# Kernel tuning notes

Hardware: AMD Instinct MI355X
Metric: run time of the kernel (lower is better)

## Reference

```python
import jax, jax.numpy as jnp
import numpy as np

HEADS = 4
DIM_HEAD = 32
SCALE = 10.0
EPS = 1e-12  # F.normalize eps


def setup_inputs() -> dict:
    key = jax.random.key(0)
    k0, k1, k2 = jax.random.split(key, 3)
    b, c, h, w = 4, 256, 64, 64
    hidden = HEADS * DIM_HEAD  # 128
    x = jax.random.normal(k0, (b, c, h, w), dtype=jnp.float32)
    # 1x1 convs == per-pixel linear layers; store as [out_ch, in_ch]
    w_qkv = jax.random.normal(k1, (3 * hidden, c), dtype=jnp.float32) * (1.0 / np.sqrt(c))
    w_out = jax.random.normal(k2, (c, hidden), dtype=jnp.float32) * (1.0 / np.sqrt(hidden))
    b_out = jnp.zeros((c,), dtype=jnp.float32)
    return {"x": x, "w_qkv": w_qkv, "w_out": w_out, "b_out": b_out}


def _l2norm(t):
    # normalize along the per-head feature dim d (axis=2 of [b,h,d,n])
    n = jnp.sqrt(jnp.sum(t * t, axis=2, keepdims=True))
    return t / jnp.maximum(n, EPS)


def reference(x, w_qkv, w_out, b_out):
    b, c, h, w = x.shape
    n = h * w
    # to_qkv 1x1 conv (no bias)
    qkv = jnp.einsum('oc,bchw->bohw', w_qkv, x)          # [b, 3*hidden, h, w]
    qkv = qkv.reshape(b, 3, HEADS, DIM_HEAD, n)          # chunk dim=1 then split heads
    q, k, v = qkv[:, 0], qkv[:, 1], qkv[:, 2]            # each [b, heads, d, n]
    q = _l2norm(q)
    k = _l2norm(k)
    sim = jnp.einsum('bhdi,bhdj->bhij', q, k) * SCALE    # [b, heads, n, n]
    attn = jax.nn.softmax(sim, axis=-1)
    out = jnp.einsum('bhij,bhdj->bhid', attn, v)         # [b, heads, n, d]
    # 'b h (x y) d -> b (h d) x y'
    out = out.transpose(0, 1, 3, 2).reshape(b, HEADS * DIM_HEAD, h, w)
    # to_out 1x1 conv with bias
    return jnp.einsum('oc,bchw->bohw', w_out, out) + b_out[None, :, None, None]
```

## Files before the change

kernel.cpp:

```cpp
#include <hip/hip_runtime.h>
#include <math.h>

#define BB 4
#define CC 256
#define NHEAD 4
#define DH 32
#define NN 4096
#define HID 128

typedef _Float16 f16;
typedef _Float16 f16x8 __attribute__((ext_vector_type(8)));
typedef _Float16 f16x4 __attribute__((ext_vector_type(4)));
typedef float f32x4 __attribute__((ext_vector_type(4)));
typedef unsigned int u32x4 __attribute__((ext_vector_type(4)));

#define QPRESCALE 14.42695041f
#define NSHIFT 14.42695041f

#if __has_builtin(__builtin_amdgcn_exp2f)
#define EXP2F(x) __builtin_amdgcn_exp2f(x)
#else
#define EXP2F(x) __expf((x)*0.6931471805599453f)
#endif

__device__ __forceinline__ f16x8 cvt8(const float* p) {
    float4 a = *(const float4*)p;
    float4 b = *(const float4*)(p + 4);
    f16x8 r;
    r[0] = (f16)a.x; r[1] = (f16)a.y; r[2] = (f16)a.z; r[3] = (f16)a.w;
    r[4] = (f16)b.x; r[5] = (f16)b.y; r[6] = (f16)b.z; r[7] = (f16)b.w;
    return r;
}

#define XROW 40

__global__ __launch_bounds__(256, 4) void qkv_mega(const float* __restrict__ x,
                                                   const float* __restrict__ wq,
                                                   f16* __restrict__ qh,
                                                   f16* __restrict__ kh,
                                                   f16* __restrict__ vh) {
    __shared__ __align__(16) f16 xl[32 * XROW];
    int t = threadIdx.x;
    int wave = t >> 6, lane = t & 63;
    int quad = lane >> 4, col = lane & 15;
    int b = blockIdx.z;
    int i0 = blockIdx.x * 32;
    int o0w = blockIdx.y * 128 + wave * 32;

    int sc = t >> 3;
    int iseg = t & 7;
    const float* xb = x + (size_t)b * CC * NN + i0 + iseg * 4;

    f32x4 c[2][2];
#pragma unroll
    for (int mt = 0; mt < 2; mt++)
#pragma unroll
        for (int nt = 0; nt < 2; nt++) c[mt][nt] = f32x4{0.f, 0.f, 0.f, 0.f};

#pragma unroll
    for (int k0 = 0; k0 < CC; k0 += 32) {
        float4 xv = *(const float4*)(xb + (size_t)(k0 + sc) * NN);
        __syncthreads();
        xl[(iseg * 4 + 0) * XROW + sc] = (f16)xv.x;
        xl[(iseg * 4 + 1) * XROW + sc] = (f16)xv.y;
        xl[(iseg * 4 + 2) * XROW + sc] = (f16)xv.z;
        xl[(iseg * 4 + 3) * XROW + sc] = (f16)xv.w;
        __syncthreads();
        f16x8 bf0 = *(const f16x8*)(xl + (size_t)col * XROW + quad * 8);
        f16x8 bf1 = *(const f16x8*)(xl + (size_t)(16 + col) * XROW + quad * 8);
#pragma unroll
        for (int mt = 0; mt < 2; mt++) {
            f16x8 a = cvt8(wq + (size_t)(o0w + mt * 16 + col) * CC + k0 + quad * 8);
            c[mt][0] = __builtin_amdgcn_mfma_f32_16x16x32_f16(a, bf0, c[mt][0], 0, 0, 0);
            c[mt][1] = __builtin_amdgcn_mfma_f32_16x16x32_f16(a, bf1, c[mt][1], 0, 0, 0);
        }
    }

    if (blockIdx.y < 2) {
        int isQ = (blockIdx.y == 0);
        f16* dst = isQ ? qh : kh;
        int h = wave;
        float pre = isQ ? QPRESCALE : 1.0f;
#pragma unroll
        for (int nt = 0; nt < 2; nt++) {
            float ss = 0.f;
#pragma unroll
            for (int m2 = 0; m2 < 2; m2++)
#pragma unroll
                for (int r = 0; r < 4; r++) {
                    float v = c[m2][nt][r];
                    ss = fmaf(v, v, ss);
                }
            ss += __shfl_xor(ss, 16);
            ss += __shfl_xor(ss, 32);
            float inv = pre / fmaxf(sqrtf(ss), 1e-12f);
            size_t row = ((size_t)(b * 4 + h) * NN + i0 + nt * 16 + col) * 32;
#pragma unroll
            for (int m2 = 0; m2 < 2; m2++) {
                f16x4 st;
#pragma unroll
                for (int r = 0; r < 4; r++) st[r] = (f16)(c[m2][nt][r] * inv);
                *(f16x4*)(dst + row + m2 * 16 + quad * 4) = st;
            }
        }
    } else {
        int h = wave;
#pragma unroll
        for (int nt = 0; nt < 2; nt++) {
            int i = i0 + nt * 16 + col;
#pragma unroll
            for (int m2 = 0; m2 < 2; m2++)
#pragma unroll
                for (int r = 0; r < 4; r++)
                    vh[((size_t)(b * 4 + h) * 32 + m2 * 16 + quad * 4 + r) * NN + i] =
                        (f16)c[m2][nt][r];
        }
    }
}

#define KROW 40
#define VROW 72

__device__ __forceinline__ f16x8 expblk2(f32x4 sa, f32x4 sb) {
    u32x4 w;
    w[0] = __builtin_bit_cast(unsigned int,
            __builtin_amdgcn_cvt_pkrtz(EXP2F(sa[0]), EXP2F(sa[1])));
    w[1] = __builtin_bit_cast(unsigned int,
            __builtin_amdgcn_cvt_pkrtz(EXP2F(sa[2]), EXP2F(sa[3])));
    w[2] = __builtin_bit_cast(unsigned int,
            __builtin_amdgcn_cvt_pkrtz(EXP2F(sb[0]), EXP2F(sb[1])));
    w[3] = __builtin_bit_cast(unsigned int,
            __builtin_amdgcn_cvt_pkrtz(EXP2F(sb[2]), EXP2F(sb[3])));
    return __builtin_bit_cast(f16x8, w);
}

__device__ __forceinline__ void compute_g(const f16* kl, const f16* vl, int jb,
                                          int col, int quad, const f16x8 (&qB)[4],
                                          f32x4 (&o)[4][2], f32x4 (&lf)[4]) {
    f16x8 kA = *(const f16x8*)(kl + (jb + col) * KROW + quad * 8);
    f16x8 kB = *(const f16x8*)(kl + (jb + 16 + col) * KROW + quad * 8);
    f16x8 v0 = *(const f16x8*)(vl + col * VROW + jb + quad * 8);
    f16x8 v1 = *(const f16x8*)(vl + (16 + col) * VROW + jb + quad * 8);
    const f32x4 zs = {-NSHIFT, -NSHIFT, -NSHIFT, -NSHIFT};
    f16 one = (f16)1.0f;
    f16x8 ones = {one, one, one, one, one, one, one, one};
#pragma unroll
    for (int f = 0; f < 4; f++) {
        f32x4 sa = __builtin_amdgcn_mfma_f32_16x16x32_f16(kA, qB[f], zs, 0, 0, 0);
        f32x4 sb = __builtin_amdgcn_mfma_f32_16x16x32_f16(kB, qB[f], zs, 0, 0, 0);
        f16x8 p = expblk2(sa, sb);
        o[f][0] = __builtin_amdgcn_mfma_f32_16x16x32_f16(p, v0, o[f][0], 0, 0, 0);
        o[f][1] = __builtin_amdgcn_mfma_f32_16x16x32_f16(p, v1, o[f][1], 0, 0, 0);
        lf[f]   = __builtin_amdgcn_mfma_f32_16x16x32_f16(p, ones, lf[f], 0, 0, 0);
    }
}

template <int SPLIT>
__global__ __launch_bounds__(256, 4) void attn_mfma(const f16* __restrict__ qh,
                                                    const f16* __restrict__ kh,
                                                    const f16* __restrict__ vh,
                                                    float* __restrict__ op,
                                                    float* __restrict__ lp,
                                                    f16* __restrict__ att16) {
    __shared__ __align__(16) f16 klds[2][64 * KROW];
    __shared__ __align__(16) f16 vlds[2][32 * VROW];
    int t = threadIdx.x;
    int wave = t >> 6, lane = t & 63;
    int quad = lane >> 4, col = lane & 15;

    int bid = blockIdx.x;
    int xcd = bid & 7;
    int slot = bid >> 3;
    int bh = xcd * 2 + slot / (16 * SPLIT);
    int rem = slot % (16 * SPLIT);
    int s = rem >> 4;
    int i0 = (rem & 15) * 256;
    int iw = i0 + wave * 64;

    const int NT = 64 / SPLIT;
    int kbase = s * (NN / SPLIT);

    const f16* qb = qh + (size_t)bh * NN * 32;
    const f16* kb = kh + (size_t)bh * NN * 32 + (size_t)kbase * 32;
    const f16* vb = vh + (size_t)bh * 32 * NN + kbase;

    f16x8 qB[4];
#pragma unroll
    for (int f = 0; f < 4; f++)
        qB[f] = *(const f16x8*)(qb + (size_t)(iw + f * 16 + col) * 32 + quad * 8);

    f32x4 o[4][2], lf[4];
#pragma unroll
    for (int f = 0; f < 4; f++) {
        o[f][0] = f32x4{0.f, 0.f, 0.f, 0.f};
        o[f][1] = f32x4{0.f, 0.f, 0.f, 0.f};
        lf[f]   = f32x4{0.f, 0.f, 0.f, 0.f};
    }

    int ktr = t >> 2, kts = t & 3;
    int ksrc = (ktr & 32) | ((ktr & 12) << 1) | ((ktr & 16) >> 2) | (ktr & 3);
    int vtr = t >> 3, vts = t & 7;

    f16x8 kr, vr;
    kr = *(const f16x8*)(kb + (size_t)(0 + ksrc) * 32 + kts * 8);
    vr = *(const f16x8*)(vb + (size_t)vtr * NN + 0 + vts * 8);
    *(f16x8*)(&klds[0][0] + ktr * KROW + kts * 8) = kr;
    *(f16x8*)(&vlds[0][0] + vtr * VROW + vts * 8) = vr;
    __syncthreads();
    kr = *(const f16x8*)(kb + (size_t)(64 + ksrc) * 32 + kts * 8);
    vr = *(const f16x8*)(vb + (size_t)vtr * NN + 64 + vts * 8);

    for (int tile = 0; tile < NT - 2; tile++) {
        int buf = tile & 1;
        const f16* kl = &klds[buf][0];
        const f16* vl = &vlds[buf][0];
        compute_g(kl, vl, 0, col, quad, qB, o, lf);
        compute_g(kl, vl, 32, col, quad, qB, o, lf);
        *(f16x8*)(&klds[buf ^ 1][0] + ktr * KROW + kts * 8) = kr;
        *(f16x8*)(&vlds[buf ^ 1][0] + vtr * VROW + vts * 8) = vr;
        __syncthreads();
        int j0 = (tile + 2) * 64;
        kr = *(const f16x8*)(kb + (size_t)(j0 + ksrc) * 32 + kts * 8);
        vr = *(const f16x8*)(vb + (size_t)vtr * NN + j0 + vts * 8);
    }
    {
        compute_g(&klds[0][0], &vlds[0][0], 0, col, quad, qB, o, lf);
        compute_g(&klds[0][0], &vlds[0][0], 32, col, quad, qB, o, lf);
        *(f16x8*)(&klds[1][0] + ktr * KROW + kts * 8) = kr;
        *(f16x8*)(&vlds[1][0] + vtr * VROW + vts * 8) = vr;
        __syncthreads();
    }
    {
        compute_g(&klds[1][0], &vlds[1][0], 0, col, quad, qB, o, lf);
        compute_g(&klds[1][0], &vlds[1][0], 32, col, quad, qB, o, lf);
    }

    if constexpr (SPLIT == 1) {
        int b = bh >> 2, h = bh & 3;
        f16* ab = att16 + (size_t)b * NN * HID + h * 32;
#pragma unroll
        for (int f = 0; f < 4; f++)
#pragma unroll
            for (int r = 0; r < 4; r++) {
                float inv = __builtin_amdgcn_rcpf(lf[f][r]);
                size_t row = (size_t)(iw + f * 16 + quad * 4 + r) * HID;
                ab[row + col]      = (f16)(o[f][0][r] * inv);
                ab[row + 16 + col] = (f16)(o[f][1][r] * inv);
            }
    } else {
        float* ob = op + (size_t)(s * 16 + bh) * NN * 32;
#pragma unroll
        for (int f = 0; f < 4; f++)
#pragma unroll
            for (int r = 0; r < 4; r++) {
                size_t rr = (size_t)(iw + f * 16 + quad * 4 + r) * 32;
                ob[rr + col]      = o[f][0][r];
                ob[rr + 16 + col] = o[f][1][r];
            }
        if (col == 0) {
            float* lb = lp + (size_t)(s * 16 + bh) * NN;
#pragma unroll
            for (int f = 0; f < 4; f++)
#pragma unroll
                for (int r = 0; r < 4; r++)
                    lb[iw + f * 16 + quad * 4 + r] = lf[f][r];
        }
    }
}

__global__ __launch_bounds__(256) void attn_combine(const float* __restrict__ op,
                                                    const float* __restrict__ lp,
                                                    f16* __restrict__ att16,
                                                    int nsplit) {
    int gid = blockIdx.x * 256 + threadIdx.x;
    int rowid = gid >> 3;
    int seg = gid & 7;
    int bh = rowid >> 12;
    int q = rowid & 4095;

    float l = 0.f;
    f32x4 acc = {0.f, 0.f, 0.f, 0.f};
    for (int s = 0; s < nsplit; s++) {
        l += lp[(size_t)(s * 16 + bh) * NN + q];
        f32x4 a = *(const f32x4*)(op + ((size_t)(s * 16 + bh) * NN + q) * 32 + seg * 4);
        acc += a;
    }
    float inv = __builtin_amdgcn_rcpf(l);
    int b = bh >> 2, h = bh & 3;
    f16x4 st;
    st[0] = (f16)(acc[0] * inv);
    st[1] = (f16)(acc[1] * inv);
    st[2] = (f16)(acc[2] * inv);
    st[3] = (f16)(acc[3] * inv);
    *(f16x4*)(att16 + ((size_t)b * NN + q) * HID + h * 32 + seg * 4) = st;
}

#define WROW 136

__global__ __launch_bounds__(256, 4) void out_mfma(const f16* __restrict__ att16,
                                                   const float* __restrict__ wo,
                                                   const float* __restrict__ bo,
                                                   float* __restrict__ out) {
    __shared__ __align__(16) f16 wol[64 * WROW];
    int t = threadIdx.x;
    int wave = t >> 6, lane = t & 63;
    int quad = lane >> 4, col = lane & 15;
    int b = blockIdx.z;
    int i0w = blockIdx.x * 64 + wave * 16;
    int o0 = blockIdx.y * 64;
    const f16* ab = att16 + (size_t)b * NN * HID;

    {
        int row = t >> 2;
        int kq = (t & 3) * 32;
        const float* src = wo + (size_t)(o0 + row) * HID + kq;
        f16* d = wol + row * WROW + kq;
#pragma unroll
        for (int j = 0; j < 4; j++) {
            float4 a = *(const float4*)(src + j * 8);
            float4 bq = *(const float4*)(src + j * 8 + 4);
            f16x8 s;
            s[0] = (f16)a.x; s[1] = (f16)a.y; s[2] = (f16)a.z; s[3] = (f16)a.w;
            s[4] = (f16)bq.x; s[5] = (f16)bq.y; s[6] = (f16)bq.z; s[7] = (f16)bq.w;
            *(f16x8*)(d + j * 8) = s;
        }
    }
    __syncthreads();

    const f32x4 z = {0.f, 0.f, 0.f, 0.f};
    f32x4 c[4];
#pragma unroll
    for (int ot = 0; ot < 4; ot++) c[ot] = z;

#pragma unroll
    for (int k0 = 0; k0 < HID; k0 += 32) {
        f16x8 a0 = *(const f16x8*)(ab + (size_t)(i0w + col) * HID + k0 + quad * 8);
#pragma unroll
        for (int ot = 0; ot < 4; ot++) {
            f16x8 bf = *(const f16x8*)(wol + (size_t)(ot * 16 + col) * WROW + k0 + quad * 8);
            c[ot] = __builtin_amdgcn_mfma_f32_16x16x32_f16(a0, bf, c[ot], 0, 0, 0);
        }
    }

#pragma unroll
    for (int ot = 0; ot < 4; ot++) {
        int o = o0 + ot * 16 + col;
        float bias = bo[o];
        int i = i0w + quad * 4;
        float4 st = {c[ot][0] + bias, c[ot][1] + bias,
                     c[ot][2] + bias, c[ot][3] + bias};
        *(float4*)(out + ((size_t)b * CC + o) * NN + i) = st;
    }
}

extern "C" void kernel_launch(void* const* d_in, const int* in_sizes, int n_in,
                              void* d_out, int out_size, void* d_ws, size_t ws_size,
                              hipStream_t stream) {
    const float* x     = (const float*)d_in[0];
    const float* w_qkv = (const float*)d_in[1];
    const float* w_out = (const float*)d_in[2];
    const float* b_out = (const float*)d_in[3];
    float* out = (float*)d_out;

    char* ws = (char*)d_ws;
    f16* qh    = (f16*)(ws);
    f16* kh    = (f16*)(ws + (4u << 20));
    f16* vh    = (f16*)(ws + (8u << 20));
    f16* att16 = (f16*)(ws + (12u << 20));

    qkv_mega<<<dim3(NN / 32, 3, BB), 256, 0, stream>>>(x, w_qkv, qh, kh, vh);

    if (ws_size >= (50ull << 20)) {
        float* op = (float*)(ws + (16ull << 20));
        float* lp = (float*)(ws + (48ull << 20));
        attn_mfma<4><<<dim3(1024), 256, 0, stream>>>(qh, kh, vh, op, lp, att16);
        attn_combine<<<dim3(2048), 256, 0, stream>>>(op, lp, att16, 4);
    } else if (ws_size >= (33ull << 20)) {
        float* op = (float*)(ws + (16ull << 20));
        float* lp = (float*)(ws + (32ull << 20));
        attn_mfma<2><<<dim3(512), 256, 0, stream>>>(qh, kh, vh, op, lp, att16);
        attn_combine<<<dim3(2048), 256, 0, stream>>>(op, lp, att16, 2);
    } else {
        attn_mfma<1><<<dim3(256), 256, 0, stream>>>(qh, kh, vh, nullptr, nullptr, att16);
    }

    out_mfma<<<dim3(NN / 64, CC / 64, BB), 256, 0, stream>>>(att16, w_out, b_out, out);
}
```

Baseline: 151.2 us.

## Fuse split-K attention combine into output projection kernel

```diff
diff --git a/kernel.cpp b/kernel.cpp
--- a/kernel.cpp
+++ b/kernel.cpp
@@ -268,34 +268,88 @@
     }
 }
 
-__global__ __launch_bounds__(256) void attn_combine(const float* __restrict__ op,
-                                                    const float* __restrict__ lp,
-                                                    f16* __restrict__ att16,
-                                                    int nsplit) {
-    int gid = blockIdx.x * 256 + threadIdx.x;
-    int rowid = gid >> 3;
-    int seg = gid & 7;
-    int bh = rowid >> 12;
-    int q = rowid & 4095;
-
-    float l = 0.f;
-    f32x4 acc = {0.f, 0.f, 0.f, 0.f};
-    for (int s = 0; s < nsplit; s++) {
-        l += lp[(size_t)(s * 16 + bh) * NN + q];
-        f32x4 a = *(const f32x4*)(op + ((size_t)(s * 16 + bh) * NN + q) * 32 + seg * 4);
-        acc += a;
-    }
-    float inv = __builtin_amdgcn_rcpf(l);
-    int b = bh >> 2, h = bh & 3;
-    f16x4 st;
-    st[0] = (f16)(acc[0] * inv);
-    st[1] = (f16)(acc[1] * inv);
-    st[2] = (f16)(acc[2] * inv);
-    st[3] = (f16)(acc[3] * inv);
-    *(f16x4*)(att16 + ((size_t)b * NN + q) * HID + h * 32 + seg * 4) = st;
-}
-
 #define WROW 136
+
+template <int NS>
+__global__ __launch_bounds__(256) void out_fused(const float* __restrict__ op,
+                                                 const float* __restrict__ lp,
+                                                 const float* __restrict__ wo,
+                                                 const float* __restrict__ bo,
+                                                 float* __restrict__ out) {
+    __shared__ __align__(16) f16 wol[128 * WROW];
+    int t = threadIdx.x;
+    int wave = t >> 6, lane = t & 63;
+    int quad = lane >> 4, col = lane & 15;
+    int b = blockIdx.z;
+    int i0w = blockIdx.x * 64 + wave * 16;
+    int o0 = blockIdx.y * 128;
+
+    {
+        int row = t >> 1;
+        int kh = (t & 1) * 64;
+        const float* src = wo + (size_t)(o0 + row) * HID + kh;
+        f16* d = wol + row * WROW + kh;
+#pragma unroll
+        for (int j = 0; j < 8; j++) {
+            float4 a = *(const float4*)(src + j * 8);
+            float4 bq = *(const float4*)(src + j * 8 + 4);
+            f16x8 s;
+            s[0] = (f16)a.x; s[1] = (f16)a.y; s[2] = (f16)a.z; s[3] = (f16)a.w;
+            s[4] = (f16)bq.x; s[5] = (f16)bq.y; s[6] = (f16)bq.z; s[7] = (f16)bq.w;
+            *(f16x8*)(d + j * 8) = s;
+        }
+    }
+    __syncthreads();
+
+    int i = i0w + col;
+    float invl[4];
+#pragma unroll
+    for (int h = 0; h < 4; h++) {
+        float l = 0.f;
+#pragma unroll
+        for (int s = 0; s < NS; s++)
+            l += lp[(size_t)(s * 16 + b * 4 + h) * NN + i];
+        invl[h] = __builtin_amdgcn_rcpf(l);
+    }
+
+    const f32x4 z = {0.f, 0.f, 0.f, 0.f};
+    f32x4 c[8];
+#pragma unroll
+    for (int ot = 0; ot < 8; ot++) c[ot] = z;
+
+#pragma unroll
+    for (int k0 = 0; k0 < HID; k0 += 32) {
+        int h = k0 >> 5;
+        f32x4 accA = z, accB = z;
+#pragma unroll
+        for (int s = 0; s < NS; s++) {
+            const float* src = op + ((size_t)(s * 16 + b * 4 + h) * NN + i) * 32 + quad * 8;
+            accA += *(const f32x4*)(src);
+            accB += *(const f32x4*)(src + 4);
+        }
+        float iv = invl[h];
+        f16x8 a0;
+        a0[0] = (f16)(accA[0] * iv); a0[1] = (f16)(accA[1] * iv);
+        a0[2] = (f16)(accA[2] * iv); a0[3] = (f16)(accA[3] * iv);
+        a0[4] = (f16)(accB[0] * iv); a0[5] = (f16)(accB[1] * iv);
+        a0[6] = (f16)(accB[2] * iv); a0[7] = (f16)(accB[3] * iv);
+#pragma unroll
+        for (int ot = 0; ot < 8; ot++) {
+            f16x8 bf = *(const f16x8*)(wol + (size_t)(ot * 16 + col) * WROW + k0 + quad * 8);
+            c[ot] = __builtin_amdgcn_mfma_f32_16x16x32_f16(a0, bf, c[ot], 0, 0, 0);
+        }
+    }
+
+#pragma unroll
+    for (int ot = 0; ot < 8; ot++) {
+        int o = o0 + ot * 16 + col;
+        float bias = bo[o];
+        int ii = i0w + quad * 4;
+        float4 st = {c[ot][0] + bias, c[ot][1] + bias,
+                     c[ot][2] + bias, c[ot][3] + bias};
+        *(float4*)(out + ((size_t)b * CC + o) * NN + ii) = st;
+    }
+}
 
 __global__ __launch_bounds__(256, 4) void out_mfma(const f16* __restrict__ att16,
                                                    const float* __restrict__ wo,
@@ -374,15 +428,14 @@
         float* op = (float*)(ws + (16ull << 20));
         float* lp = (float*)(ws + (48ull << 20));
         attn_mfma<4><<<dim3(1024), 256, 0, stream>>>(qh, kh, vh, op, lp, att16);
-        attn_combine<<<dim3(2048), 256, 0, stream>>>(op, lp, att16, 4);
+        out_fused<4><<<dim3(NN / 64, 2, BB), 256, 0, stream>>>(op, lp, w_out, b_out, out);
     } else if (ws_size >= (33ull << 20)) {
         float* op = (float*)(ws + (16ull << 20));
         float* lp = (float*)(ws + (32ull << 20));
         attn_mfma<2><<<dim3(512), 256, 0, stream>>>(qh, kh, vh, op, lp, att16);
-        attn_combine<<<dim3(2048), 256, 0, stream>>>(op, lp, att16, 2);
+        out_fused<2><<<dim3(NN / 64, 2, BB), 256, 0, stream>>>(op, lp, w_out, b_out, out);
     } else {
         attn_mfma<1><<<dim3(256), 256, 0, stream>>>(qh, kh, vh, nullptr, nullptr, att16);
-    }
-
-    out_mfma<<<dim3(NN / 64, CC / 64, BB), 256, 0, stream>>>(att16, w_out, b_out, out);
-}
+        out_mfma<<<dim3(NN / 64, CC / 64, BB), 256, 0, stream>>>(att16, w_out, b_out, out);
+    }
+}
```

Measured after the change: 152.0 us. No clear change (+0.6%).
